# Kernel optimization log

Hardware: AMD Instinct MI355X
Metric: run time of the kernel (lower is better)

Reference implementation:

```python
import jax, jax.numpy as jnp
import numpy as np

PIXELSIZE = 65.0   # nm per pixel (sim_params().pixelsize)
TWO_PI = 2.0 * np.pi


def sf_modulation(xyz, mod, roipos):
    # xyz: [B,3], mod: [B,F,6] (kx,ky,kz,depth,phase,relint), roipos: [B,2]
    k = mod[..., :3]          # [B,F,3]
    depth = mod[..., 3]       # [B,F]
    phase = mod[..., 4]       # [B,F]
    relint = mod[..., 5]      # [B,F]
    xyz_mod = xyz.at[:, :2].set(roipos + xyz[:, :2])
    em_phase = jnp.mod((xyz_mod[:, None, :] * k).sum(-1), TWO_PI) - phase  # [B,F]
    deriv = (depth * jnp.cos(em_phase) * relint)[..., None] * k            # [B,F,3]
    intensity = (1.0 + depth * jnp.sin(em_phase)) * relint                 # [B,F]
    return intensity, deriv


def setup_inputs() -> dict:
    key = jax.random.key(0)
    k0, k1, k2, k3, k4, k5, k6 = jax.random.split(key, 7)
    B, F, M = 16384, 6, 16
    # params = [x, y, z, I, bg] with realistic localization-microscopy scales
    xy = 8.0 + jax.random.normal(k0, (B, 2), jnp.float32)          # near ROI center
    z = 0.1 * jax.random.normal(k1, (B, 1), jnp.float32)
    I = 1000.0 + 100.0 * jax.random.normal(k2, (B, 1), jnp.float32)
    bg = 20.0 + jax.random.uniform(k3, (B, 1), jnp.float32)
    params = jnp.concatenate([xy, z, I, bg], axis=-1)               # [B,5]
    # mod: kx,ky,kz ~ O(1) rad/px, depth in (0,1), phase in [0,2pi), relint ~ 1/F
    kvec = jax.random.uniform(k4, (B, F, 3), jnp.float32, 0.5, 2.0)
    depth = jax.random.uniform(k4, (B, F, 1), jnp.float32, 0.7, 1.0)
    phase = jax.random.uniform(k5, (B, F, 1), jnp.float32, 0.0, TWO_PI)
    relint = jnp.full((B, F, 1), 1.0 / F, jnp.float32)
    mod = jnp.concatenate([kvec, depth, phase, relint], axis=-1)    # [B,F,6]
    roipos = jnp.floor(jax.random.uniform(k5, (B, 2), jnp.float32, 0.0, 512.0))
    psf_ev = jax.random.uniform(k6, (B, M, M), jnp.float32) * 0.02  # [B,Mx,My]
    psf_deriv = 0.01 * jax.random.normal(k6, (B, M, M, 5), jnp.float32)
    return {"params": params, "mod": mod, "roipos": roipos,
            "psf_ev": psf_ev, "psf_deriv": psf_deriv}


def reference(params, mod, roipos, psf_ev, psf_deriv):
    xyz = params[:, :3]
    I = params[:, 3]
    bg = params[:, 4]
    mod_intensity, mod_deriv = sf_modulation(xyz, mod, roipos)      # [B,F], [B,F,3]
    # unit conversion applied to PSF derivatives (x,y: /pixelsize, z: /1000)
    scale = jnp.array([1.0 / PIXELSIZE, 1.0 / PIXELSIZE, 1e-3, 1.0, 1.0],
                      psf_deriv.dtype)
    pd = psf_deriv * scale                                          # [B,Mx,My,5]
    phot = I[:, None, None, None]                                   # [B,1,1,1]
    # mu: [B,F,Mx,My]
    mu = bg[:, None, None, None] + mod_intensity[:, :, None, None] * phot * psf_ev[:, None]
    # deriv_xyz: [B,F,Mx,My,3]
    deriv_xyz = phot[..., None] * (
        mod_deriv[:, :, None, None, :] * psf_ev[:, None, :, :, None]
        + mod_intensity[:, :, None, None, None] * pd[:, None, :, :, :3])
    deriv_I = psf_ev[:, None] * mod_intensity[:, :, None, None]     # [B,F,Mx,My]
    deriv_bg = jnp.ones_like(deriv_I)
    deriv = jnp.concatenate(
        [deriv_xyz, deriv_I[..., None], deriv_bg[..., None]], axis=-1)  # [B,F,Mx,My,5]
    return mu, deriv
```

## Files before the change

### kernel.cpp

```cpp
#include <hip/hip_runtime.h>
#include <math.h>

#define NF 6
#define M2 256
#define TWO_PI_F 6.283185307179586f

__global__ __launch_bounds__(256) void simflux_kernel(
    const float* __restrict__ params,
    const float* __restrict__ mod,
    const float* __restrict__ roipos,
    const float* __restrict__ psf_ev,
    const float* __restrict__ psf_deriv,
    float* __restrict__ out_mu,
    float* __restrict__ out_deriv)
{
    const unsigned b = blockIdx.x;
    const unsigned t = threadIdx.x;

    __shared__ float ev_s[M2];
    __shared__ float pd_s[M2 * 5];
    __shared__ float A_s[NF][5];
    __shared__ float Bc_s[NF][5];
    __shared__ float S_s[NF];

    ev_s[t] = psf_ev[b * M2 + t];
    const float* pdb = psf_deriv + (size_t)b * (M2 * 5);
    #pragma unroll
    for (int i = 0; i < 5; ++i) pd_s[i * 256 + t] = pdb[i * 256 + t];

    const float x   = params[b * 5 + 0];
    const float y   = params[b * 5 + 1];
    const float z   = params[b * 5 + 2];
    const float Iph = params[b * 5 + 3];
    const float bg  = params[b * 5 + 4];

    if (t < NF) {
        const unsigned f = t;
        const float rx = roipos[b * 2 + 0];
        const float ry = roipos[b * 2 + 1];
        const float* mf = mod + ((size_t)b * NF + f) * 6;
        const float k0 = mf[0], k1 = mf[1], k2 = mf[2];
        const float depth = mf[3], phase = mf[4], relint = mf[5];

        float dot = (x + rx) * k0 + (y + ry) * k1 + z * k2;
        float r = fmodf(dot, TWO_PI_F);
        if (r < 0.f) r += TWO_PI_F;
        const float em = r - phase;
        const float sn = sinf(em);
        const float cs = cosf(em);

        const float intensity = (1.f + depth * sn) * relint;
        const float dcr = depth * cs * relint;
        const float sI  = Iph * intensity;

        A_s[f][0] = Iph * dcr * k0;
        A_s[f][1] = Iph * dcr * k1;
        A_s[f][2] = Iph * dcr * k2;
        A_s[f][3] = intensity;
        A_s[f][4] = 0.f;
        Bc_s[f][0] = sI * (1.0f / 65.0f);
        Bc_s[f][1] = sI * (1.0f / 65.0f);
        Bc_s[f][2] = sI * 0.001f;
        Bc_s[f][3] = 0.f;
        Bc_s[f][4] = 0.f;
        S_s[f] = sI;
    }
    __syncthreads();

    float2* mu2 = (float2*)(out_mu + (size_t)b * (NF * M2));
    #pragma unroll
    for (int j = 0; j < 3; ++j) {
        const unsigned q = j * 256 + t;
        const unsigned f = q >> 7;
        const unsigned p = (q & 127u) * 2u;
        const float s = S_s[f];
        float2 v;
        v.x = bg + s * ev_s[p];
        v.y = bg + s * ev_s[p + 1];
        mu2[q] = v;
    }

    float2* dv2 = (float2*)(out_deriv + (size_t)b * (NF * M2 * 5));
    #pragma unroll
    for (int j = 0; j < 15; ++j) {
        const unsigned q = j * 256 + t;
        const unsigned f = q / 640u;
        const unsigned e = (q * 2u) % 1280u;
        const unsigned p = e / 5u;
        const unsigned c = e - p * 5u;
        unsigned c1 = c + 1u;
        unsigned p1 = p;
        if (c1 == 5u) { c1 = 0u; p1 = p + 1u; }

        float v0 = A_s[f][c]  * ev_s[p]  + Bc_s[f][c]  * pd_s[e]     + (c  == 4u ? 1.f : 0.f);
        float v1 = A_s[f][c1] * ev_s[p1] + Bc_s[f][c1] * pd_s[e + 1] + (c1 == 4u ? 1.f : 0.f);
        float2 v; v.x = v0; v.y = v1;
        dv2[q] = v;
    }
}

extern "C" void kernel_launch(void* const* d_in, const int* in_sizes, int n_in,
                              void* d_out, int out_size, void* d_ws, size_t ws_size,
                              hipStream_t stream) {
    const float* params    = (const float*)d_in[0];
    const float* mod       = (const float*)d_in[1];
    const float* roipos    = (const float*)d_in[2];
    const float* psf_ev    = (const float*)d_in[3];
    const float* psf_deriv = (const float*)d_in[4];

    const int B = in_sizes[0] / 5;
    const size_t mu_elems = (size_t)B * NF * M2;

    float* out_mu    = (float*)d_out;
    float* out_deriv = (float*)d_out + mu_elems;

    simflux_kernel<<<B, 256, 0, stream>>>(params, mod, roipos, psf_ev, psf_deriv,
                                          out_mu, out_deriv);
}
```

Baseline: 655.5 us.

## Compute derivs per pixel in registers, stage through LDS, store float4

Each thread now reads only the three psf_deriv components it needs (skipping the I/bg components) and computes its pixel's five derivative values per frame. It writes them to a double-buffered LDS tile and then copies the tile out with coalesced float4 stores. The mu output also moves to float4 stores. This removes the per-element div/mod index arithmetic and the full staging of psf_deriv, at the cost of one barrier per frame and strided global loads of pd.

```diff
diff --git a/kernel.cpp b/kernel.cpp
--- a/kernel.cpp
+++ b/kernel.cpp
@@ -17,28 +17,27 @@
     const unsigned b = blockIdx.x;
     const unsigned t = threadIdx.x;
 
-    __shared__ float ev_s[M2];
-    __shared__ float pd_s[M2 * 5];
-    __shared__ float A_s[NF][5];
-    __shared__ float Bc_s[NF][5];
-    __shared__ float S_s[NF];
+    __shared__ __align__(16) float ev_s[M2];
+    __shared__ __align__(16) float d_s[2][M2 * 5];
+    __shared__ float coef_s[NF][8];
 
-    ev_s[t] = psf_ev[b * M2 + t];
-    const float* pdb = psf_deriv + (size_t)b * (M2 * 5);
-    #pragma unroll
-    for (int i = 0; i < 5; ++i) pd_s[i * 256 + t] = pdb[i * 256 + t];
+    ev_s[t] = psf_ev[(size_t)b * M2 + t];
 
-    const float x   = params[b * 5 + 0];
-    const float y   = params[b * 5 + 1];
-    const float z   = params[b * 5 + 2];
-    const float Iph = params[b * 5 + 3];
-    const float bg  = params[b * 5 + 4];
+    const float* pdt = psf_deriv + (size_t)b * (M2 * 5) + t * 5u;
+    const float pd0 = pdt[0];
+    const float pd1 = pdt[1];
+    const float pd2 = pdt[2];
+
+    const float bg = params[b * 5u + 4u];
 
     if (t < NF) {
-        const unsigned f = t;
+        const float x   = params[b * 5 + 0];
+        const float y   = params[b * 5 + 1];
+        const float z   = params[b * 5 + 2];
+        const float Iph = params[b * 5 + 3];
         const float rx = roipos[b * 2 + 0];
         const float ry = roipos[b * 2 + 1];
-        const float* mf = mod + ((size_t)b * NF + f) * 6;
+        const float* mf = mod + ((size_t)b * NF + t) * 6;
         const float k0 = mf[0], k1 = mf[1], k2 = mf[2];
         const float depth = mf[3], phase = mf[4], relint = mf[5];
 
@@ -53,49 +52,52 @@
         const float dcr = depth * cs * relint;
         const float sI  = Iph * intensity;
 
-        A_s[f][0] = Iph * dcr * k0;
-        A_s[f][1] = Iph * dcr * k1;
-        A_s[f][2] = Iph * dcr * k2;
-        A_s[f][3] = intensity;
-        A_s[f][4] = 0.f;
-        Bc_s[f][0] = sI * (1.0f / 65.0f);
-        Bc_s[f][1] = sI * (1.0f / 65.0f);
-        Bc_s[f][2] = sI * 0.001f;
-        Bc_s[f][3] = 0.f;
-        Bc_s[f][4] = 0.f;
-        S_s[f] = sI;
+        coef_s[t][0] = Iph * dcr * k0;
+        coef_s[t][1] = Iph * dcr * k1;
+        coef_s[t][2] = Iph * dcr * k2;
+        coef_s[t][3] = intensity;
+        coef_s[t][4] = sI * (1.0f / 65.0f);
+        coef_s[t][5] = sI * (1.0f / 65.0f);
+        coef_s[t][6] = sI * 0.001f;
+        coef_s[t][7] = sI;
     }
     __syncthreads();
 
-    float2* mu2 = (float2*)(out_mu + (size_t)b * (NF * M2));
-    #pragma unroll
-    for (int j = 0; j < 3; ++j) {
-        const unsigned q = j * 256 + t;
-        const unsigned f = q >> 7;
-        const unsigned p = (q & 127u) * 2u;
-        const float s = S_s[f];
-        float2 v;
-        v.x = bg + s * ev_s[p];
-        v.y = bg + s * ev_s[p + 1];
-        mu2[q] = v;
+    float4* mu4 = (float4*)(out_mu + (size_t)b * (NF * M2));
+    const float4* ev4 = (const float4*)ev_s;
+    {
+        unsigned f = t >> 6, p = t & 63u;
+        float4 e = ev4[p];
+        float s = coef_s[f][7];
+        mu4[t] = make_float4(bg + s * e.x, bg + s * e.y, bg + s * e.z, bg + s * e.w);
+        if (t < 128u) {
+            const unsigned q = 256u + t;
+            f = q >> 6; p = q & 63u;
+            e = ev4[p]; s = coef_s[f][7];
+            mu4[q] = make_float4(bg + s * e.x, bg + s * e.y, bg + s * e.z, bg + s * e.w);
+        }
     }
 
-    float2* dv2 = (float2*)(out_deriv + (size_t)b * (NF * M2 * 5));
+    const float evt = ev_s[t];
+    float4* dv4 = (float4*)(out_deriv + (size_t)b * (NF * M2 * 5));
     #pragma unroll
-    for (int j = 0; j < 15; ++j) {
-        const unsigned q = j * 256 + t;
-        const unsigned f = q / 640u;
-        const unsigned e = (q * 2u) % 1280u;
-        const unsigned p = e / 5u;
-        const unsigned c = e - p * 5u;
-        unsigned c1 = c + 1u;
-        unsigned p1 = p;
-        if (c1 == 5u) { c1 = 0u; p1 = p + 1u; }
-
-        float v0 = A_s[f][c]  * ev_s[p]  + Bc_s[f][c]  * pd_s[e]     + (c  == 4u ? 1.f : 0.f);
-        float v1 = A_s[f][c1] * ev_s[p1] + Bc_s[f][c1] * pd_s[e + 1] + (c1 == 4u ? 1.f : 0.f);
-        float2 v; v.x = v0; v.y = v1;
-        dv2[q] = v;
+    for (int f = 0; f < NF; ++f) {
+        float* dd = d_s[f & 1];
+        const float v0 = coef_s[f][0] * evt + coef_s[f][4] * pd0;
+        const float v1 = coef_s[f][1] * evt + coef_s[f][5] * pd1;
+        const float v2 = coef_s[f][2] * evt + coef_s[f][6] * pd2;
+        const float v3 = coef_s[f][3] * evt;
+        const unsigned base = t * 5u;
+        dd[base + 0] = v0;
+        dd[base + 1] = v1;
+        dd[base + 2] = v2;
+        dd[base + 3] = v3;
+        dd[base + 4] = 1.0f;
+        __syncthreads();
+        const float4* d4 = (const float4*)dd;
+        float4* dst = dv4 + f * (M2 * 5 / 4);
+        dst[t] = d4[t];
+        if (t < 64u) dst[256u + t] = d4[256u + t];
     }
 }
 
```

After: 658.2 us. About the same (+0.4%).
